# Performance work log

Measured on AMD Instinct MI355X. Metric: run time of the kernel, lower is better.

Reference implementation:

```python
import jax, jax.numpy as jnp
import numpy as np

B, C, H, W = 16, 512, 64, 64
WS = 16            # window size -> N = 256 tokens per window
NH = 16            # num heads, head_dim = 32
HD = C // NH
HID = int((4 * C * 0.5) / 64) * 64   # SwiGLU hidden = 1024
CPB = 512
EPS = 1e-5


def _rel_tables(ws):
    r = np.arange(-(ws - 1), ws, dtype=np.float32)
    tab = np.stack(np.meshgrid(r, r, indexing='ij'), axis=-1)  # (2ws-1,2ws-1,2)
    tab = tab / (ws - 1)
    tab = tab * 8.0
    tab = np.sign(tab) * np.log2(np.abs(tab) + 1.0) / np.log2(8.0)
    # relative position index (N,N)
    coords = np.stack(np.meshgrid(np.arange(ws), np.arange(ws), indexing='ij'))
    cf = coords.reshape(2, -1)
    rel = (cf[:, :, None] - cf[:, None, :]).transpose(1, 2, 0).astype(np.int64)
    rel[:, :, 0] += ws - 1
    rel[:, :, 1] += ws - 1
    rel[:, :, 0] *= 2 * ws - 1
    idx = rel.sum(-1)
    return tab.reshape(-1, 2), idx


def setup_inputs() -> dict:
    key = jax.random.key(0)
    ks = jax.random.split(key, 12)
    s = 0.02
    tab, idx = _rel_tables(WS)
    return {
        'x': jax.random.normal(ks[0], (B, C, H, W), jnp.float32),
        'rel_table': jnp.asarray(tab),
        'norm1_w': jnp.ones((C,), jnp.float32),
        'norm1_b': jnp.zeros((C,), jnp.float32),
        'norm2_w': jnp.ones((C,), jnp.float32),
        'norm2_b': jnp.zeros((C,), jnp.float32),
        'qkv_w': jax.random.normal(ks[1], (C, 3 * C), jnp.float32) * s,
        'proj_w': jax.random.normal(ks[2], (C, C), jnp.float32) * s,
        'cpb_w1': jax.random.normal(ks[3], (2, CPB), jnp.float32) * s,
        'cpb_b1': jnp.zeros((CPB,), jnp.float32),
        'cpb_w2': jax.random.normal(ks[4], (CPB, NH), jnp.float32) * s,
        'fc1_w': jax.random.normal(ks[5], (C, 2 * HID), jnp.float32) * s,
        'fc2_w': jax.random.normal(ks[6], (HID, C), jnp.float32) * s,
        'rel_index': jnp.asarray(idx),
    }


def _ln(x, w, b):
    m = jnp.mean(x, axis=-1, keepdims=True)
    v = jnp.mean(jnp.square(x - m), axis=-1, keepdims=True)
    return (x - m) * jax.lax.rsqrt(v + EPS) * w + b


def reference(x, rel_table, norm1_w, norm1_b, norm2_w, norm2_b, qkv_w, proj_w,
              cpb_w1, cpb_b1, cpb_w2, fc1_w, fc2_w, rel_index):
    ws, nh, hd = WS, NH, HD
    N = ws * ws
    # window partition: (B,C,H,W) -> (B*nW, N, C)
    xw = x.reshape(B, C, H // ws, ws, W // ws, ws)
    xw = xw.transpose(0, 2, 4, 3, 5, 1).reshape(-1, N, C)
    Bw = xw.shape[0]

    # --- window attention ---
    h = _ln(xw, norm1_w, norm1_b)
    qkv = (h @ qkv_w).reshape(Bw, N, 3, nh, hd).transpose(2, 0, 3, 1, 4)
    q, k, v = qkv[0], qkv[1], qkv[2]          # (Bw, nh, N, hd)
    attn = jnp.einsum('bhnd,bhmd->bhnm', q, k) * (hd ** -0.5)
    # Swin-v2 continuous position bias MLP + gather
    bias_tab = jax.nn.relu(rel_table @ cpb_w1 + cpb_b1) @ cpb_w2   # ((2ws-1)^2, nh)
    bias = bias_tab[rel_index]                 # (N, N, nh)
    bias = 16.0 * jax.nn.sigmoid(bias.transpose(2, 0, 1))          # (nh, N, N)
    attn = jax.nn.softmax(attn + bias[None], axis=-1)
    o = jnp.einsum('bhnm,bhmd->bhnd', attn, v)
    o = o.transpose(0, 2, 1, 3).reshape(Bw, N, C) @ proj_w
    xw = xw + o

    # --- SwiGLU MLP ---
    h2 = _ln(xw, norm2_w, norm2_b)
    u = h2 @ fc1_w
    val, gate = jnp.split(u, 2, axis=-1)       # Mlp/SwiGLU: chunk -> silu(gate)*x
    xw = xw + (jax.nn.silu(gate) * val) @ fc2_w

    # window reverse + outer skip
    xr = xw.reshape(B, H // ws, W // ws, ws, ws, C)
    xr = xr.transpose(0, 5, 1, 3, 2, 4).reshape(B, C, H, W)
    return xr + x
```

## Files before the change

### kernel.cpp

```cpp
#include <hip/hip_runtime.h>
#include <hip/hip_bf16.h>

typedef unsigned short u16;
typedef unsigned int u32;
typedef __attribute__((ext_vector_type(8))) u16 u16x8;
typedef __attribute__((ext_vector_type(4))) u16 u16x4;
typedef __attribute__((ext_vector_type(8))) short bf16x8;
typedef __attribute__((ext_vector_type(4))) float f32x4;

__device__ __forceinline__ u16 f2bf(float f) {
  u32 u = __float_as_uint(f);
  u += 0x7fffu + ((u >> 16) & 1u);
  return (u16)(u >> 16);
}
__device__ __forceinline__ float bf2f(u16 h) {
  return __uint_as_float(((u32)h) << 16);
}
__device__ __forceinline__ u16 cvt_bf(float f) {
  __hip_bfloat16 h(f);
  return __builtin_bit_cast(u16, h);
}
__device__ __forceinline__ bf16x8 ld_bf8(const u16* p) {
  return __builtin_bit_cast(bf16x8, *(const u16x8*)p);
}

#if __has_builtin(__builtin_amdgcn_exp2f)
#define EXP2(x) __builtin_amdgcn_exp2f(x)
#else
#define EXP2(x) exp2f(x)
#endif

typedef const void __attribute__((address_space(1)))* gas_t;
typedef void __attribute__((address_space(3)))* las_t;
#define GLOAD_LDS16(gp, lp) __builtin_amdgcn_global_load_lds((gas_t)(gp), (las_t)(lp), 16, 0, 0)

#define QSCALE 0.25503486f
#define BIAS_MUL 23.08312065f

__global__ void prep_kernel(
    const float* __restrict__ qkv_w, const float* __restrict__ proj_w,
    const float* __restrict__ fc1_w, const float* __restrict__ fc2_w,
    const float* __restrict__ rt, const float* __restrict__ cw1,
    const float* __restrict__ cb1, const float* __restrict__ cw2,
    u16* __restrict__ wq, u16* __restrict__ wp, u16* __restrict__ w1,
    u16* __restrict__ w2, float* __restrict__ tab2) {
  int b = blockIdx.x, t = threadIdx.x;
  if (b < 3072) {
    int idx = b * 256 + t;
    int n = idx >> 9, k = idx & 511;
    float s = n < 512 ? QSCALE : 1.f;
    wq[idx] = f2bf(qkv_w[(size_t)k * 1536 + n] * s);
  } else if (b < 4096) {
    int idx = (b - 3072) * 256 + t;
    int n = idx >> 9, k = idx & 511;
    wp[idx] = f2bf(proj_w[(size_t)k * 512 + n]);
  } else if (b < 8192) {
    int idx = (b - 4096) * 256 + t;
    int n = idx >> 9, k = idx & 511;
    int i = ((n >> 5) << 4) | (n & 15);
    int gsel = (n >> 4) & 1;
    w1[idx] = f2bf(fc1_w[(size_t)k * 2048 + i + gsel * 1024]);
  } else if (b < 10240) {
    int idx = (b - 8192) * 256 + t;
    int n = idx >> 10, k = idx & 1023;
    w2[idx] = f2bf(fc2_w[(size_t)k * 512 + n]);
  } else {
    __shared__ float hid[512];
    __shared__ float part[16][17];
    int tix = b - 10240;
    float r0 = rt[tix * 2], r1 = rt[tix * 2 + 1];
    for (int j = t; j < 512; j += 256) {
      float v = r0 * cw1[j] + r1 * cw1[512 + j] + cb1[j];
      hid[j] = v > 0.f ? v : 0.f;
    }
    __syncthreads();
    int hh = t & 15, seg = t >> 4;
    float acc = 0.f;
    for (int j = seg * 32; j < seg * 32 + 32; ++j) acc += hid[j] * cw2[j * 16 + hh];
    part[seg][hh] = acc;
    __syncthreads();
    if (t < 16) {
      float s = 0.f;
      for (int g = 0; g < 16; ++g) s += part[g][t];
      tab2[t * 961 + tix] = BIAS_MUL / (1.f + __expf(-s)) - 23.0f;
    }
  }
}

__global__ __launch_bounds__(256, 4) void ln1_kernel(
    const float* __restrict__ x, const float* __restrict__ w, const float* __restrict__ b,
    u16* __restrict__ hbuf, u16* __restrict__ xwbuf) {
  __shared__ u16 tile[512 * 33];
  __shared__ float red[2][8][32];
  __shared__ float meanv[32], rstdv[32];
  int bi = blockIdx.x;
  int bimg = bi >> 7, rest = bi & 127, hrow = rest >> 1, half = rest & 1;
  int t = threadIdx.x, p = t & 31, g = t >> 5;
  const float* xr = x + (size_t)bimg * 512 * 4096 + (size_t)hrow * 64 + half * 32;
  float s = 0.f, s2 = 0.f;
  for (int i = 0; i < 64; ++i) {
    int c = g * 64 + i;
    float v = xr[(size_t)c * 4096 + p];
    tile[c * 33 + p] = f2bf(v);
    s += v; s2 += v * v;
  }
  red[0][g][p] = s; red[1][g][p] = s2;
  __syncthreads();
  if (t < 32) {
    float ss = 0.f, qq = 0.f;
    for (int gg = 0; gg < 8; ++gg) { ss += red[0][gg][t]; qq += red[1][gg][t]; }
    float mu = ss * (1.f / 512.f);
    float var = qq * (1.f / 512.f) - mu * mu;
    meanv[t] = mu;
    rstdv[t] = rsqrtf(var + 1e-5f);
  }
  __syncthreads();
  int c0 = t * 2;
  float w0 = w[c0], w1v = w[c0 + 1], b0 = b[c0], b1v = b[c0 + 1];
  int hy = hrow >> 4, iy = hrow & 15;
  for (int pp = 0; pp < 32; ++pp) {
    int pixel = half * 32 + pp;
    int wx = pixel >> 4, ix = pixel & 15;
    int widx = bimg * 16 + hy * 4 + wx;
    size_t basep = ((size_t)widx * 256 + iy * 16 + ix) * 512;
    u16 rb0 = tile[c0 * 33 + pp], rb1 = tile[(c0 + 1) * 33 + pp];
    float mu = meanv[pp], rs = rstdv[pp];
    float v0 = bf2f(rb0), v1 = bf2f(rb1);
    *(u32*)(xwbuf + basep + c0) = (u32)rb0 | ((u32)rb1 << 16);
    u16 h0 = f2bf((v0 - mu) * rs * w0 + b0);
    u16 h1 = f2bf((v1 - mu) * rs * w1v + b1v);
    *(u32*)(hbuf + basep + c0) = (u32)h0 | ((u32)h1 << 16);
  }
}

template <int EPI>
__global__ __launch_bounds__(256, 4) void gemm_bt(
    const u16* __restrict__ A, const u16* __restrict__ Bt,
    u16* __restrict__ out, const u16* __restrict__ res,
    const float* __restrict__ xg, float* __restrict__ outf,
    int M, int N, int K) {
  __shared__ u16 As[128 * 64];
  __shared__ u16 Bs[128 * 64];
  const int t = threadIdx.x, l = t & 63, wv = t >> 6;
  const int nbx = N >> 7;
  const int wg = (int)blockIdx.x;
  const int xcd = wg & 7, c = wg >> 3;
  const int cm = c / nbx;
  const int m0 = (xcd * 64 + cm) * 128, n0 = (c - cm * nbx) * 128;
  const int wr = wv >> 1, wc = wv & 1;
  const int lr = l & 15, lk = l >> 4;
  f32x4 acc[4][4] = {};
  for (int kt = 0; kt < K; kt += 64) {
#pragma unroll
    for (int j = 0; j < 4; ++j) {
      int qi = j * 256 + t;
      int r = qi >> 3, c8 = (qi & 7) * 8;
      GLOAD_LDS16(A + (size_t)(m0 + r) * K + kt + c8, As + (size_t)(j * 256 + wv * 64) * 8);
    }
#pragma unroll
    for (int j = 0; j < 4; ++j) {
      int qi = j * 256 + t;
      int r = qi >> 3, c8 = (qi & 7) * 8;
      GLOAD_LDS16(Bt + (size_t)(n0 + r) * K + kt + c8, Bs + (size_t)(j * 256 + wv * 64) * 8);
    }
    __syncthreads();
#pragma unroll
    for (int ks = 0; ks < 2; ++ks) {
      bf16x8 a[4], bb[4];
#pragma unroll
      for (int mf = 0; mf < 4; ++mf)
        a[mf] = ld_bf8(As + (wr * 64 + mf * 16 + lr) * 64 + ks * 32 + lk * 8);
#pragma unroll
      for (int nf = 0; nf < 4; ++nf)
        bb[nf] = ld_bf8(Bs + (wc * 64 + nf * 16 + lr) * 64 + ks * 32 + lk * 8);
#pragma unroll
      for (int mf = 0; mf < 4; ++mf)
#pragma unroll
        for (int nf = 0; nf < 4; ++nf)
          acc[mf][nf] = __builtin_amdgcn_mfma_f32_16x16x32_bf16(a[mf], bb[nf], acc[mf][nf], 0, 0, 0);
    }
    __syncthreads();
  }
#pragma unroll
  for (int mf = 0; mf < 4; ++mf) {
    int rbase = m0 + wr * 64 + mf * 16 + lk * 4;
    if constexpr (EPI == 3) {
#pragma unroll
      for (int nf = 0; nf < 4; nf += 2) {
        int colv = n0 + wc * 64 + nf * 16 + lr;
        int i = ((colv >> 5) << 4) | (colv & 15);
#pragma unroll
        for (int jj = 0; jj < 4; ++jj) {
          int row = rbase + jj;
          float val = acc[mf][nf][jj], gate = acc[mf][nf + 1][jj];
          float sil = gate / (1.f + __expf(-gate));
          out[(size_t)row * 1024 + i] = f2bf(sil * val);
        }
      }
    } else if constexpr (EPI == 4) {
      int widx = rbase >> 8, iy = (rbase >> 4) & 15, ix0 = rbase & 15;
      int bimg = widx >> 4, hy = (widx >> 2) & 3, wx = widx & 3;
#pragma unroll
      for (int nf = 0; nf < 4; ++nf) {
        int col = n0 + wc * 64 + nf * 16 + lr;
        size_t obase = (((size_t)(bimg * 512 + col) * 64) + hy * 16 + iy) * 64 + wx * 16 + ix0;
        const float* xp = xg + obase;
        float* op = outf + obase;
#pragma unroll
        for (int jj = 0; jj < 4; ++jj)
          op[jj] = acc[mf][nf][jj] + bf2f(res[(size_t)(rbase + jj) * 512 + col]) + xp[jj];
      }
    } else if constexpr (EPI == 1) {
#pragma unroll
      for (int nf = 0; nf < 4; ++nf) {
        int col = n0 + wc * 64 + nf * 16 + lr;
#pragma unroll
        for (int jj = 0; jj < 4; ++jj) {
          int row = rbase + jj;
          out[(size_t)row * N + col] = f2bf(acc[mf][nf][jj] + bf2f(res[(size_t)row * N + col]));
        }
      }
    } else {
#pragma unroll
      for (int nf = 0; nf < 4; ++nf) {
        int col = n0 + wc * 64 + nf * 16 + lr;
#pragma unroll
        for (int jj = 0; jj < 4; ++jj)
          out[(size_t)(rbase + jj) * N + col] = f2bf(acc[mf][nf][jj]);
      }
    }
  }
}

__global__ __launch_bounds__(256, 4) void attn_kernel(
    const u16* __restrict__ qkv, const float* __restrict__ tab2, u16* __restrict__ ob) {
  __shared__ u16 vt[32 * 72];
  __shared__ float tabh4[31 * 32 * 4];
  __shared__ u16 pl[4][16 * 76];
  const int h = blockIdx.x, w = blockIdx.y;
  const int t = threadIdx.x, l = t & 63, wid = t >> 6;
  const u16* qg = qkv + (size_t)(w * 256) * 1536 + h * 32;
  const u16* kg = qg + 512;
  const u16* vg = qg + 1024;
  const float* th = tab2 + h * 961;
  for (int i = t; i < 992; i += 256) {
    int dy = i >> 5, dx = i & 31;
#pragma unroll
    for (int r = 0; r < 4; ++r) {
      int dxr = dx + r;
      tabh4[i * 4 + r] = (dxr <= 30) ? th[dy * 31 + dxr] : 0.f;
    }
  }
  const int q4 = l >> 4, c0 = l & 15;
  const int dx0 = q4 * 4 - c0 + 15;
  bf16x8 qa[4];
#pragma unroll
  for (int mf = 0; mf < 4; ++mf)
    qa[mf] = ld_bf8(qg + (size_t)(wid * 64 + mf * 16 + c0) * 1536 + q4 * 8);
  f32x4 oacc[4][2] = {};
  float psum[4][4] = {};
  for (int ct = 0; ct < 4; ++ct) {
    {
      int r = t & 63, j = t >> 6;
      u16x8 dv = *(const u16x8*)(vg + (size_t)(ct * 64 + r) * 1536 + j * 8);
#pragma unroll
      for (int e = 0; e < 8; ++e) vt[(j * 8 + e) * 72 + r] = dv[e];
    }
    __syncthreads();
    bf16x8 bfr[4];
#pragma unroll
    for (int nf = 0; nf < 4; ++nf)
      bfr[nf] = ld_bf8(kg + (size_t)(ct * 64 + nf * 16 + c0) * 1536 + q4 * 8);
    bf16x8 vfr[2][2];
#pragma unroll
    for (int df = 0; df < 2; ++df)
#pragma unroll
      for (int ks2 = 0; ks2 < 2; ++ks2)
        vfr[df][ks2] = ld_bf8(vt + (df * 16 + c0) * 72 + ks2 * 32 + q4 * 8);
#pragma unroll
    for (int mf = 0; mf < 4; ++mf) {
      const int dyb = wid * 4 + mf - ct * 4 + 15;
      f32x4 sacc[4];
#pragma unroll
      for (int nf = 0; nf < 4; ++nf)
        sacc[nf] = *(const f32x4*)&tabh4[((dyb - nf) * 32 + dx0) * 4];
      __builtin_amdgcn_s_setprio(1);
#pragma unroll
      for (int nf = 0; nf < 4; ++nf)
        sacc[nf] = __builtin_amdgcn_mfma_f32_16x16x32_bf16(qa[mf], bfr[nf], sacc[nf], 0, 0, 0);
      __builtin_amdgcn_s_setprio(0);
#pragma unroll
      for (int nf = 0; nf < 4; ++nf) {
#pragma unroll
        for (int jj = 0; jj < 4; ++jj) {
          float p = EXP2(sacc[nf][jj]);
          psum[mf][jj] += p;
          pl[wid][(q4 * 4 + jj) * 76 + nf * 16 + c0] = cvt_bf(p);
        }
      }
      __builtin_amdgcn_s_setprio(1);
#pragma unroll
      for (int ks2 = 0; ks2 < 2; ++ks2) {
        bf16x8 pa = ld_bf8(&pl[wid][c0 * 76 + ks2 * 32 + q4 * 8]);
        oacc[mf][0] = __builtin_amdgcn_mfma_f32_16x16x32_bf16(pa, vfr[0][ks2], oacc[mf][0], 0, 0, 0);
        oacc[mf][1] = __builtin_amdgcn_mfma_f32_16x16x32_bf16(pa, vfr[1][ks2], oacc[mf][1], 0, 0, 0);
      }
      __builtin_amdgcn_s_setprio(0);
    }
    __syncthreads();
  }
#pragma unroll
  for (int mf = 0; mf < 4; ++mf) {
#pragma unroll
    for (int jj = 0; jj < 4; ++jj) {
      float s = psum[mf][jj];
      s += __shfl_xor(s, 1);
      s += __shfl_xor(s, 2);
      s += __shfl_xor(s, 4);
      s += __shfl_xor(s, 8);
      float inv = 1.f / s;
      int row = wid * 64 + mf * 16 + q4 * 4 + jj;
      size_t obase = ((size_t)w * 256 + row) * 512 + h * 32;
      ob[obase + c0] = f2bf(oacc[mf][0][jj] * inv);
      ob[obase + 16 + c0] = f2bf(oacc[mf][1][jj] * inv);
    }
  }
}

__global__ __launch_bounds__(256, 4) void ln2_kernel(const u16* __restrict__ r1,
    const float* __restrict__ w, const float* __restrict__ b, u16* __restrict__ h2) {
  int t = threadIdx.x, l = t & 63, wid = t >> 6;
  size_t token = (size_t)blockIdx.x * 4 + wid;
  const u16* rp = r1 + token * 512 + l * 8;
  u16x8 raw = *(const u16x8*)rp;
  float v[8]; float s = 0.f, s2 = 0.f;
#pragma unroll
  for (int i = 0; i < 8; ++i) { v[i] = bf2f(raw[i]); s += v[i]; s2 += v[i] * v[i]; }
#pragma unroll
  for (int m = 1; m < 64; m <<= 1) { s += __shfl_xor(s, m); s2 += __shfl_xor(s2, m); }
  float mu = s * (1.f / 512.f);
  float var = s2 * (1.f / 512.f) - mu * mu;
  float rs = rsqrtf(var + 1e-5f);
  u16x8 o;
#pragma unroll
  for (int i = 0; i < 8; ++i) {
    int c = l * 8 + i;
    o[i] = f2bf((v[i] - mu) * rs * w[c] + b[c]);
  }
  *(u16x8*)(h2 + token * 512 + l * 8) = o;
}

extern "C" void kernel_launch(void* const* d_in, const int* in_sizes, int n_in,
                              void* d_out, int out_size, void* d_ws, size_t ws_size,
                              hipStream_t stream) {
  (void)in_sizes; (void)n_in; (void)out_size; (void)ws_size;
  const float* x = (const float*)d_in[0];
  const float* rel_table = (const float*)d_in[1];
  const float* n1w = (const float*)d_in[2];
  const float* n1b = (const float*)d_in[3];
  const float* n2w = (const float*)d_in[4];
  const float* n2b = (const float*)d_in[5];
  const float* qkv_w = (const float*)d_in[6];
  const float* proj_w = (const float*)d_in[7];
  const float* cpb_w1 = (const float*)d_in[8];
  const float* cpb_b1 = (const float*)d_in[9];
  const float* cpb_w2 = (const float*)d_in[10];
  const float* fc1_w = (const float*)d_in[11];
  const float* fc2_w = (const float*)d_in[12];
  float* outp = (float*)d_out;
  char* ws = (char*)d_ws;

  u16* wq = (u16*)(ws + 0);
  u16* wp = (u16*)(ws + 1572864);
  u16* w1 = (u16*)(ws + 2097152);
  u16* w2 = (u16*)(ws + 4194304);
  float* tab2 = (float*)(ws + 5242880);
  const size_t RB = 67108864;
  u16* R0 = (u16*)(ws + 8388608);
  u16* R1 = (u16*)(ws + 8388608 + RB);
  u16* R2 = (u16*)(ws + 8388608 + 2 * RB);
  u16* R3 = (u16*)(ws + 8388608 + 3 * RB);
  u16* R4 = (u16*)(ws + 8388608 + 4 * RB);

  prep_kernel<<<11201, 256, 0, stream>>>(qkv_w, proj_w, fc1_w, fc2_w,
                                         rel_table, cpb_w1, cpb_b1, cpb_w2,
                                         wq, wp, w1, w2, tab2);
  ln1_kernel<<<2048, 256, 0, stream>>>(x, n1w, n1b, R2, R0);
  gemm_bt<0><<<6144, 256, 0, stream>>>(R2, wq, R3, nullptr,
                                       nullptr, nullptr, 65536, 1536, 512);
  attn_kernel<<<dim3(16, 256), 256, 0, stream>>>(R3, tab2, R2);
  gemm_bt<1><<<2048, 256, 0, stream>>>(R2, wp, R1, R0,
                                       nullptr, nullptr, 65536, 512, 512);
  ln2_kernel<<<16384, 256, 0, stream>>>(R1, n2w, n2b, R3);
  gemm_bt<3><<<8192, 256, 0, stream>>>(R3, w1, R4, nullptr,
                                       nullptr, nullptr, 65536, 2048, 512);
  gemm_bt<4><<<2048, 256, 0, stream>>>(R4, w2, nullptr, R1,
                                       x, outp, 65536, 512, 1024);
}
```

Baseline: 746.9 us.

## Merge weight prep into LN1 kernel and double-buffer V tiles in attention

Folds the weight-conversion/bias-table prep kernel and the LN1 windowing kernel into one launch, with the prep branch reusing the LN tile shared memory. In the attention kernel, V tiles are now double-buffered: the next chunk is loaded from global into registers before the MFMA loop and written to the alternate LDS buffer afterward, which removes the trailing barrier per iteration. This saves one launch and overlaps V loads with compute, at the cost of extra LDS. The prep blocks also now carry the LN kernel's larger shared-memory footprint and 4-blocks-per-CU launch bound, which could lower their occupancy.

```diff
diff --git a/kernel.cpp b/kernel.cpp
--- a/kernel.cpp
+++ b/kernel.cpp
@@ -37,14 +37,61 @@
 #define QSCALE 0.25503486f
 #define BIAS_MUL 23.08312065f
 
-__global__ void prep_kernel(
+__global__ __launch_bounds__(256, 4) void head_kernel(
+    const float* __restrict__ x, const float* __restrict__ n1w, const float* __restrict__ n1b,
+    u16* __restrict__ hbuf, u16* __restrict__ xwbuf,
     const float* __restrict__ qkv_w, const float* __restrict__ proj_w,
     const float* __restrict__ fc1_w, const float* __restrict__ fc2_w,
     const float* __restrict__ rt, const float* __restrict__ cw1,
     const float* __restrict__ cb1, const float* __restrict__ cw2,
     u16* __restrict__ wq, u16* __restrict__ wp, u16* __restrict__ w1,
     u16* __restrict__ w2, float* __restrict__ tab2) {
-  int b = blockIdx.x, t = threadIdx.x;
+  __shared__ u16 tile[512 * 33];
+  __shared__ float red[2][8][32];
+  __shared__ float meanv[32], rstdv[32];
+  int blk = blockIdx.x, t = threadIdx.x;
+  if (blk < 2048) {
+    int bi = blk;
+    int bimg = bi >> 7, rest = bi & 127, hrow = rest >> 1, half = rest & 1;
+    int p = t & 31, g = t >> 5;
+    const float* xr = x + (size_t)bimg * 512 * 4096 + (size_t)hrow * 64 + half * 32;
+    float s = 0.f, s2 = 0.f;
+    for (int i = 0; i < 64; ++i) {
+      int c = g * 64 + i;
+      float v = xr[(size_t)c * 4096 + p];
+      tile[c * 33 + p] = f2bf(v);
+      s += v; s2 += v * v;
+    }
+    red[0][g][p] = s; red[1][g][p] = s2;
+    __syncthreads();
+    if (t < 32) {
+      float ss = 0.f, qq = 0.f;
+      for (int gg = 0; gg < 8; ++gg) { ss += red[0][gg][t]; qq += red[1][gg][t]; }
+      float mu = ss * (1.f / 512.f);
+      float var = qq * (1.f / 512.f) - mu * mu;
+      meanv[t] = mu;
+      rstdv[t] = rsqrtf(var + 1e-5f);
+    }
+    __syncthreads();
+    int c0 = t * 2;
+    float w0 = n1w[c0], w1v = n1w[c0 + 1], b0 = n1b[c0], b1v = n1b[c0 + 1];
+    int hy = hrow >> 4, iy = hrow & 15;
+    for (int pp = 0; pp < 32; ++pp) {
+      int pixel = half * 32 + pp;
+      int wx = pixel >> 4, ix = pixel & 15;
+      int widx = bimg * 16 + hy * 4 + wx;
+      size_t basep = ((size_t)widx * 256 + iy * 16 + ix) * 512;
+      u16 rb0 = tile[c0 * 33 + pp], rb1 = tile[(c0 + 1) * 33 + pp];
+      float mu = meanv[pp], rs = rstdv[pp];
+      float v0 = bf2f(rb0), v1 = bf2f(rb1);
+      *(u32*)(xwbuf + basep + c0) = (u32)rb0 | ((u32)rb1 << 16);
+      u16 h0 = f2bf((v0 - mu) * rs * w0 + b0);
+      u16 h1 = f2bf((v1 - mu) * rs * w1v + b1v);
+      *(u32*)(hbuf + basep + c0) = (u32)h0 | ((u32)h1 << 16);
+    }
+    return;
+  }
+  int b = blk - 2048;
   if (b < 3072) {
     int idx = b * 256 + t;
     int n = idx >> 9, k = idx & 511;
@@ -65,8 +112,8 @@
     int n = idx >> 10, k = idx & 1023;
     w2[idx] = f2bf(fc2_w[(size_t)k * 512 + n]);
   } else {
-    __shared__ float hid[512];
-    __shared__ float part[16][17];
+    float* hid = (float*)tile;
+    float (*part)[17] = (float (*)[17])(tile + 4096);
     int tix = b - 10240;
     float r0 = rt[tix * 2], r1 = rt[tix * 2 + 1];
     for (int j = t; j < 512; j += 256) {
@@ -84,52 +131,6 @@
       for (int g = 0; g < 16; ++g) s += part[g][t];
       tab2[t * 961 + tix] = BIAS_MUL / (1.f + __expf(-s)) - 23.0f;
     }
-  }
-}
-
-__global__ __launch_bounds__(256, 4) void ln1_kernel(
-    const float* __restrict__ x, const float* __restrict__ w, const float* __restrict__ b,
-    u16* __restrict__ hbuf, u16* __restrict__ xwbuf) {
-  __shared__ u16 tile[512 * 33];
-  __shared__ float red[2][8][32];
-  __shared__ float meanv[32], rstdv[32];
-  int bi = blockIdx.x;
-  int bimg = bi >> 7, rest = bi & 127, hrow = rest >> 1, half = rest & 1;
-  int t = threadIdx.x, p = t & 31, g = t >> 5;
-  const float* xr = x + (size_t)bimg * 512 * 4096 + (size_t)hrow * 64 + half * 32;
-  float s = 0.f, s2 = 0.f;
-  for (int i = 0; i < 64; ++i) {
-    int c = g * 64 + i;
-    float v = xr[(size_t)c * 4096 + p];
-    tile[c * 33 + p] = f2bf(v);
-    s += v; s2 += v * v;
-  }
-  red[0][g][p] = s; red[1][g][p] = s2;
-  __syncthreads();
-  if (t < 32) {
-    float ss = 0.f, qq = 0.f;
-    for (int gg = 0; gg < 8; ++gg) { ss += red[0][gg][t]; qq += red[1][gg][t]; }
-    float mu = ss * (1.f / 512.f);
-    float var = qq * (1.f / 512.f) - mu * mu;
-    meanv[t] = mu;
-    rstdv[t] = rsqrtf(var + 1e-5f);
-  }
-  __syncthreads();
-  int c0 = t * 2;
-  float w0 = w[c0], w1v = w[c0 + 1], b0 = b[c0], b1v = b[c0 + 1];
-  int hy = hrow >> 4, iy = hrow & 15;
-  for (int pp = 0; pp < 32; ++pp) {
-    int pixel = half * 32 + pp;
-    int wx = pixel >> 4, ix = pixel & 15;
-    int widx = bimg * 16 + hy * 4 + wx;
-    size_t basep = ((size_t)widx * 256 + iy * 16 + ix) * 512;
-    u16 rb0 = tile[c0 * 33 + pp], rb1 = tile[(c0 + 1) * 33 + pp];
-    float mu = meanv[pp], rs = rstdv[pp];
-    float v0 = bf2f(rb0), v1 = bf2f(rb1);
-    *(u32*)(xwbuf + basep + c0) = (u32)rb0 | ((u32)rb1 << 16);
-    u16 h0 = f2bf((v0 - mu) * rs * w0 + b0);
-    u16 h1 = f2bf((v1 - mu) * rs * w1v + b1v);
-    *(u32*)(hbuf + basep + c0) = (u32)h0 | ((u32)h1 << 16);
   }
 }
 
@@ -234,7 +235,7 @@
 
 __global__ __launch_bounds__(256, 4) void attn_kernel(
     const u16* __restrict__ qkv, const float* __restrict__ tab2, u16* __restrict__ ob) {
-  __shared__ u16 vt[32 * 72];
+  __shared__ u16 vt[2][32 * 72];
   __shared__ float tabh4[31 * 32 * 4];
   __shared__ u16 pl[4][16 * 76];
   const int h = blockIdx.x, w = blockIdx.y;
@@ -243,6 +244,12 @@
   const u16* kg = qg + 512;
   const u16* vg = qg + 1024;
   const float* th = tab2 + h * 961;
+  const int vr = t & 63, vj = t >> 6;
+  {
+    u16x8 dv0 = *(const u16x8*)(vg + (size_t)vr * 1536 + vj * 8);
+#pragma unroll
+    for (int e = 0; e < 8; ++e) vt[0][(vj * 8 + e) * 72 + vr] = dv0[e];
+  }
   for (int i = t; i < 992; i += 256) {
     int dy = i >> 5, dx = i & 31;
 #pragma unroll
@@ -260,23 +267,20 @@
   f32x4 oacc[4][2] = {};
   float psum[4][4] = {};
   for (int ct = 0; ct < 4; ++ct) {
-    {
-      int r = t & 63, j = t >> 6;
-      u16x8 dv = *(const u16x8*)(vg + (size_t)(ct * 64 + r) * 1536 + j * 8);
-#pragma unroll
-      for (int e = 0; e < 8; ++e) vt[(j * 8 + e) * 72 + r] = dv[e];
-    }
     __syncthreads();
     bf16x8 bfr[4];
 #pragma unroll
     for (int nf = 0; nf < 4; ++nf)
       bfr[nf] = ld_bf8(kg + (size_t)(ct * 64 + nf * 16 + c0) * 1536 + q4 * 8);
+    const u16* vcur = vt[ct & 1];
     bf16x8 vfr[2][2];
 #pragma unroll
     for (int df = 0; df < 2; ++df)
 #pragma unroll
       for (int ks2 = 0; ks2 < 2; ++ks2)
-        vfr[df][ks2] = ld_bf8(vt + (df * 16 + c0) * 72 + ks2 * 32 + q4 * 8);
+        vfr[df][ks2] = ld_bf8(vcur + (df * 16 + c0) * 72 + ks2 * 32 + q4 * 8);
+    u16x8 dv = {};
+    if (ct < 3) dv = *(const u16x8*)(vg + (size_t)((ct + 1) * 64 + vr) * 1536 + vj * 8);
 #pragma unroll
     for (int mf = 0; mf < 4; ++mf) {
       const int dyb = wid * 4 + mf - ct * 4 + 15;
@@ -307,7 +311,10 @@
       }
       __builtin_amdgcn_s_setprio(0);
     }
-    __syncthreads();
+    if (ct < 3) {
+#pragma unroll
+      for (int e = 0; e < 8; ++e) vt[(ct + 1) & 1][(vj * 8 + e) * 72 + vr] = dv[e];
+    }
   }
 #pragma unroll
   for (int mf = 0; mf < 4; ++mf) {
@@ -382,10 +389,10 @@
   u16* R3 = (u16*)(ws + 8388608 + 3 * RB);
   u16* R4 = (u16*)(ws + 8388608 + 4 * RB);
 
-  prep_kernel<<<11201, 256, 0, stream>>>(qkv_w, proj_w, fc1_w, fc2_w,
+  head_kernel<<<13249, 256, 0, stream>>>(x, n1w, n1b, R2, R0,
+                                         qkv_w, proj_w, fc1_w, fc2_w,
                                          rel_table, cpb_w1, cpb_b1, cpb_w2,
                                          wq, wp, w1, w2, tab2);
-  ln1_kernel<<<2048, 256, 0, stream>>>(x, n1w, n1b, R2, R0);
   gemm_bt<0><<<6144, 256, 0, stream>>>(R2, wq, R3, nullptr,
                                        nullptr, nullptr, 65536, 1536, 512);
   attn_kernel<<<dim3(16, 256), 256, 0, stream>>>(R3, tab2, R2);
```

Result: slower. 801.3 us (+7.3%).
